# Kernel optimization log

Hardware: AMD Instinct MI355X
Metric: run time of the kernel (lower is better)

## Reference

```python
import math
import jax, jax.numpy as jnp
import numpy as np

CH = 256
NUM_GROUPS = 32
EPS = 1e-5


def setup_inputs() -> dict:
    key = jax.random.key(0)
    ks = jax.random.split(key, 8)
    B, C, S = 32, CH, 32
    x = jax.random.normal(ks[0], (B, C, S, S), dtype=jnp.float32)
    t_embd = jax.random.normal(ks[1], (B, 4 * C), dtype=jnp.float32)
    gamma = jnp.ones((C,), dtype=jnp.float32)
    beta = jnp.zeros((C,), dtype=jnp.float32)
    # torch nn.Linear(ch, 3*ch): weight shape (3*ch, ch), y = x @ W.T + b
    w_attn = jax.random.normal(ks[2], (3 * C, C), dtype=jnp.float32) * (1.0 / math.sqrt(C))
    b_attn = jax.random.normal(ks[3], (3 * C,), dtype=jnp.float32) * 0.02
    w_proj = jax.random.normal(ks[4], (C, C), dtype=jnp.float32) * (1.0 / math.sqrt(C))
    b_proj = jax.random.normal(ks[5], (C,), dtype=jnp.float32) * 0.02
    return {
        "x": x, "t_embd": t_embd,
        "gamma": gamma, "beta": beta,
        "w_attn": w_attn, "b_attn": b_attn,
        "w_proj": w_proj, "b_proj": b_proj,
    }


def _group_norm(x, gamma, beta):
    # x: (B, C, S, S), normalize over (C/G, S, S) per group
    B, C, S, _ = x.shape
    xg = x.reshape(B, NUM_GROUPS, (C // NUM_GROUPS) * S * S)
    mean = jnp.mean(xg, axis=-1, keepdims=True)
    var = jnp.var(xg, axis=-1, keepdims=True)
    xn = ((xg - mean) * jax.lax.rsqrt(var + EPS)).reshape(B, C, S, S)
    return xn * gamma[None, :, None, None] + beta[None, :, None, None]


def reference(x, t_embd, gamma, beta, w_attn, b_attn, w_proj, b_proj):
    B, C, S, _ = x.shape
    norm_x = _group_norm(x, gamma, beta)
    h = jnp.transpose(norm_x, (0, 2, 3, 1))            # (B, S, S, C)
    qkv = h @ w_attn.T + b_attn                        # (B, S, S, 3C)
    q, k, v = jnp.split(qkv, 3, axis=3)
    # full spatial attention: scores over all S*S key positions
    att = jnp.einsum('bhwc,bHWc->bhwHW', q, k) * (1.0 / math.sqrt(C))
    att = jax.nn.softmax(att.reshape(B, S, S, S * S), axis=-1).reshape(B, S, S, S, S)
    o = jnp.einsum('bhwHW,bHWc->bhwc', att, v)         # (B, S, S, C)
    y = o @ w_proj.T + b_proj
    y = jnp.transpose(y, (0, 3, 1, 2))                 # (B, C, S, S)
    return x + y
```

## Files before the change

kernel.cpp:

```cpp
#include <hip/hip_runtime.h>
#include <hip/hip_bf16.h>
#include <stdint.h>
#include <stddef.h>


typedef float  f32x4  __attribute__((ext_vector_type(4)));
typedef __bf16 bf16x8 __attribute__((ext_vector_type(8)));
typedef __bf16 bf16x4 __attribute__((ext_vector_type(4)));

#define DEVI static __device__ __forceinline__

DEVI f32x4 mfma16(bf16x8 a, bf16x8 b, f32x4 c) {
  return __builtin_amdgcn_mfma_f32_16x16x32_bf16(a, b, c, 0, 0, 0);
}

DEVI f32x4 zero4() { f32x4 z = {0.f, 0.f, 0.f, 0.f}; return z; }

typedef const __attribute__((address_space(1))) void* gas_cvp;
typedef __attribute__((address_space(3))) void*       las_vp;

DEVI void gl_lds16(const __bf16* g, __bf16* l) {
  __builtin_amdgcn_global_load_lds((gas_cvp)g, (las_vp)l, 16, 0, 0);
}

__global__ __launch_bounds__(256) void cvt_weights(
    const float* __restrict__ wa, const float* __restrict__ wp,
    __bf16* __restrict__ wab, __bf16* __restrict__ wpb) {
  const int i = blockIdx.x * 256 + threadIdx.x;
  if (i < 196608) {
    wab[i] = (__bf16)wa[i];
  } else {
    const int j = i - 196608;
    if (j < 65536) wpb[j] = (__bf16)wp[j];
  }
}

__global__ __launch_bounds__(256) void gn_stats(
    const float* __restrict__ x, float* __restrict__ mean, float* __restrict__ rstd) {
  const int bg = blockIdx.x;
  const f32x4* base = (const f32x4*)(x + (size_t)bg * 8192);
  float s = 0.f, ss = 0.f;
  for (int i = threadIdx.x; i < 2048; i += 256) {
    f32x4 v = base[i];
    s  += v[0] + v[1] + v[2] + v[3];
    ss += v[0]*v[0] + v[1]*v[1] + v[2]*v[2] + v[3]*v[3];
  }
#pragma unroll
  for (int m = 1; m < 64; m <<= 1) {
    s  += __shfl_xor(s,  m, 64);
    ss += __shfl_xor(ss, m, 64);
  }
  __shared__ float red[8];
  const int lane = threadIdx.x & 63, wave = threadIdx.x >> 6;
  if (lane == 0) { red[wave] = s; red[wave + 4] = ss; }
  __syncthreads();
  if (threadIdx.x == 0) {
    float S  = red[0] + red[1] + red[2] + red[3];
    float SS = red[4] + red[5] + red[6] + red[7];
    float mu  = S * (1.f / 8192.f);
    float var = SS * (1.f / 8192.f) - mu * mu;
    mean[bg] = mu;
    rstd[bg] = rsqrtf(var + 1e-5f);
  }
}

__global__ __launch_bounds__(256) void gn_apply(
    const float* __restrict__ x, const float* __restrict__ mean,
    const float* __restrict__ rstd, const float* __restrict__ gamma,
    const float* __restrict__ beta, __bf16* __restrict__ h) {
  __shared__ __align__(16) __bf16 tile[256 * 64];
  const int b = blockIdx.x >> 4;
  const int p0 = (blockIdx.x & 15) << 6;
  const int tid = threadIdx.x;
#pragma unroll
  for (int it = 0; it < 16; ++it) {
    const int ch = it * 256 + tid;
    const int c = ch >> 4, p4 = ch & 15;
    f32x4 v = *(const f32x4*)(x + (((size_t)(b * 256 + c)) << 10) + p0 + p4 * 4);
    const int bg = b * 32 + (c >> 3);
    const float rs = rstd[bg];
    const float ga = gamma[c] * rs;
    const float be = beta[c] - mean[bg] * ga;
    bf16x4 pk;
#pragma unroll
    for (int r = 0; r < 4; ++r) pk[r] = (__bf16)(v[r] * ga + be);
    *(bf16x4*)((char*)tile + c * 128 + ((p4 * 8) ^ ((c & 7) << 4))) = pk;
  }
  __syncthreads();
  const int p = tid & 63;
#pragma unroll
  for (int it = 0; it < 8; ++it) {
    const int cg = (tid >> 6) * 8 + it;
    bf16x8 vals;
#pragma unroll
    for (int jj = 0; jj < 8; ++jj) {
      const int c = cg * 8 + jj;
      vals[jj] = *(const __bf16*)((const char*)tile + c * 128 + ((p * 2) ^ (jj << 4)));
    }
    *(bf16x8*)(h + (((size_t)(b * 1024 + p0 + p)) << 8) + cg * 8) = vals;
  }
}

DEVI void gemm_core_k256(const __bf16* __restrict__ A0, const __bf16* __restrict__ B0,
                         __bf16* lA, __bf16* lB, int lane, int wave, f32x4 acc[4][4]) {
  const int wm = (wave >> 1) * 64;
  const int wn = (wave & 1) * 64;
  const int r15 = lane & 15, lg = lane >> 4;
#pragma unroll
  for (int i = 0; i < 4; ++i)
#pragma unroll
    for (int j = 0; j < 4; ++j) acc[i][j] = zero4();

  for (int ko = 0; ko < 4; ++ko) {
#pragma unroll
    for (int it = 0; it < 4; ++it) {
      const int q = wave * 256 + it * 64 + lane;
      const int row = q >> 3, c8 = q & 7;
      const int srcoff = row * 256 + ko * 64 + ((c8 ^ (row & 7)) << 3);
      gl_lds16(A0 + srcoff, lA + (size_t)(wave * 256 + it * 64) * 8);
      gl_lds16(B0 + srcoff, lB + (size_t)(wave * 256 + it * 64) * 8);
    }
    __syncthreads();
#pragma unroll
    for (int kk = 0; kk < 2; ++kk) {
      bf16x8 af[4], bfr[4];
#pragma unroll
      for (int i = 0; i < 4; ++i) {
        const int row = wm + i * 16 + r15;
        af[i] = *(const bf16x8*)((const char*)lA + row * 128 +
                                 (((kk * 4 + lg) ^ (row & 7)) << 4));
      }
#pragma unroll
      for (int j = 0; j < 4; ++j) {
        const int row = wn + j * 16 + r15;
        bfr[j] = *(const bf16x8*)((const char*)lB + row * 128 +
                                  (((kk * 4 + lg) ^ (row & 7)) << 4));
      }
#pragma unroll
      for (int i = 0; i < 4; ++i)
#pragma unroll
        for (int j = 0; j < 4; ++j) acc[i][j] = mfma16(af[i], bfr[j], acc[i][j]);
    }
    __syncthreads();
  }
}

__global__ __launch_bounds__(256) void qkv_gemm(
    const __bf16* __restrict__ h, const __bf16* __restrict__ wab,
    const float* __restrict__ b_attn,
    __bf16* __restrict__ q, __bf16* __restrict__ k, __bf16* __restrict__ vt) {
  __shared__ __align__(16) __bf16 lA[128 * 64], lB[128 * 64];
  const int nt = blockIdx.x, mt = blockIdx.y;
  const int tid = threadIdx.x, lane = tid & 63, wave = tid >> 6;
  f32x4 acc[4][4];
  gemm_core_k256(h + (size_t)mt * 128 * 256, wab + (size_t)nt * 128 * 256,
                 lA, lB, lane, wave, acc);

  const int wm = (wave >> 1) * 64, wn = (wave & 1) * 64;
  const int r15 = lane & 15, lg = lane >> 4;
  const int sec = nt >> 1;
  const float QS = 0.0625f * 1.44269504088896340736f;
#pragma unroll
  for (int j = 0; j < 4; ++j) {
    const int ng = nt * 128 + wn + j * 16 + r15;
    const float bias = b_attn[ng];
    const int c = ng & 255;
#pragma unroll
    for (int i = 0; i < 4; ++i) {
      const int mbase = mt * 128 + wm + i * 16 + lg * 4;
      if (sec == 0) {
#pragma unroll
        for (int r = 0; r < 4; ++r)
          q[(size_t)(mbase + r) * 256 + c] = (__bf16)((acc[i][j][r] + bias) * QS);
      } else if (sec == 1) {
#pragma unroll
        for (int r = 0; r < 4; ++r)
          k[(size_t)(mbase + r) * 256 + c] = (__bf16)(acc[i][j][r] + bias);
      } else {
        const int b = mbase >> 10, p = mbase & 1023;
        bf16x4 pk;
#pragma unroll
        for (int r = 0; r < 4; ++r) pk[r] = (__bf16)(acc[i][j][r] + bias);
        *(bf16x4*)(vt + (((size_t)(b * 256 + c)) << 10) + p) = pk;
      }
    }
  }
}

__global__ __launch_bounds__(256, 2) void attn(
    const __bf16* __restrict__ q, const __bf16* __restrict__ k,
    const __bf16* __restrict__ vt, __bf16* __restrict__ o) {
  extern __shared__ __align__(16) char smem[];
  __bf16* lK = (__bf16*)smem;
  __bf16* lV = (__bf16*)(smem + 32768);

  const int bid = blockIdx.x;
  const int xcd = bid & 7, sub = bid >> 3;
  const int b = xcd * 4 + (sub & 3);
  const int qt = sub >> 2;
  const int tid = threadIdx.x, lane = tid & 63, wave = tid >> 6;
  const int r15 = lane & 15, lg = lane >> 4, rs7 = r15 & 7;
  const int m0 = qt * 64 + wave * 16;
  char* P = smem + 65536 + wave * 2048;

  const __bf16* kb = k  + ((size_t)b << 18);
  const __bf16* vb = vt + ((size_t)b << 18);

  const __bf16* qb = q + (((size_t)(b * 1024 + m0)) << 8);
  bf16x8 qf[8];
#pragma unroll
  for (int kc = 0; kc < 8; ++kc)
    qf[kc] = *(const bf16x8*)(qb + ((size_t)r15) * 256 + kc * 32 + lg * 8);

  f32x4 po[16];
#pragma unroll
  for (int d = 0; d < 16; ++d) po[d] = zero4();
  float mrun[4] = {-1e30f, -1e30f, -1e30f, -1e30f};
  float lrun[4] = {0.f, 0.f, 0.f, 0.f};

  auto stageK = [&](int n0) {
#pragma unroll
    for (int it = 0; it < 8; ++it) {
      const int qch = it * 256 + tid;
      const int row = qch >> 5, c32 = qch & 31;
      gl_lds16(kb + (size_t)(n0 + row) * 256 + ((c32 ^ (row & 7)) << 3),
               lK + (size_t)(it * 256 + wave * 64) * 8);
    }
  };
  auto stageV = [&](int n0) {
#pragma unroll
    for (int it = 0; it < 8; ++it) {
      const int qch = it * 256 + tid;
      const int row = qch >> 3, c8 = qch & 7;
      gl_lds16(vb + ((size_t)row << 10) + n0 + ((c8 ^ (row & 7)) << 3),
               lV + (size_t)(it * 256 + wave * 64) * 8);
    }
  };

  stageK(0);
  stageV(0);
  __syncthreads();

  for (int kv = 0; kv < 16; ++kv) {
    const int n0n = (kv + 1) * 64;
    f32x4 s[4];
#pragma unroll
    for (int j = 0; j < 4; ++j) s[j] = zero4();
#pragma unroll
    for (int kc = 0; kc < 8; ++kc) {
      bf16x8 bfr[4];
#pragma unroll
      for (int j = 0; j < 4; ++j)
        bfr[j] = *(const bf16x8*)((const char*)lK + (j * 16 + r15) * 512 +
                                  (((kc * 4 + lg) ^ rs7) << 4));
#pragma unroll
      for (int j = 0; j < 4; ++j) s[j] = mfma16(qf[kc], bfr[j], s[j]);
    }
    float scl[4];
#pragma unroll
    for (int r = 0; r < 4; ++r) {
      float mx = fmaxf(fmaxf(s[0][r], s[1][r]), fmaxf(s[2][r], s[3][r]));
#pragma unroll
      for (int mm = 1; mm < 16; mm <<= 1) mx = fmaxf(mx, __shfl_xor(mx, mm, 64));
      const float mn = fmaxf(mrun[r], mx);
      scl[r] = exp2f(mrun[r] - mn);
      mrun[r] = mn;
    }
#pragma unroll
    for (int j = 0; j < 4; ++j)
#pragma unroll
      for (int r = 0; r < 4; ++r) s[j][r] = exp2f(s[j][r] - mrun[r]);
#pragma unroll
    for (int r = 0; r < 4; ++r) {
      float t = s[0][r] + s[1][r] + s[2][r] + s[3][r];
#pragma unroll
      for (int mm = 1; mm < 16; mm <<= 1) t += __shfl_xor(t, mm, 64);
      lrun[r] = lrun[r] * scl[r] + t;
    }
#pragma unroll
    for (int d = 0; d < 16; ++d)
#pragma unroll
      for (int r = 0; r < 4; ++r) po[d][r] *= scl[r];
#pragma unroll
    for (int j = 0; j < 4; ++j)
#pragma unroll
      for (int r = 0; r < 4; ++r) {
        const int prow = lg * 4 + r;
        *(__bf16*)(P + prow * 128 + (((j * 16 + r15) * 2) ^ ((prow & 7) << 4))) =
            (__bf16)s[j][r];
      }
    __syncthreads();
    if (kv < 15) stageK(n0n);
#pragma unroll
    for (int kk = 0; kk < 2; ++kk) {
      const bf16x8 pa =
          *(const bf16x8*)(P + r15 * 128 + (((kk * 4 + lg) ^ rs7) << 4));
#pragma unroll
      for (int df = 0; df < 16; ++df) {
        const bf16x8 vf = *(const bf16x8*)((const char*)lV + (df * 16 + r15) * 128 +
                                           (((kk * 4 + lg) ^ rs7) << 4));
        po[df] = mfma16(pa, vf, po[df]);
      }
    }
    __syncthreads();
    if (kv < 15) stageV(n0n);
  }
  __bf16* ob = o + (((size_t)(b * 1024 + m0)) << 8);
#pragma unroll
  for (int r = 0; r < 4; ++r) {
    const float inv = 1.f / lrun[r];
#pragma unroll
    for (int df = 0; df < 16; ++df)
      ob[(size_t)(lg * 4 + r) * 256 + df * 16 + r15] = (__bf16)(po[df][r] * inv);
  }
}

__global__ __launch_bounds__(256) void proj_gemm(
    const __bf16* __restrict__ o, const __bf16* __restrict__ wpb,
    const float* __restrict__ b_proj, const float* __restrict__ x,
    float* __restrict__ out) {
  __shared__ __align__(16) __bf16 lA[128 * 64], lB[128 * 64];
  const int nt = blockIdx.x, mt = blockIdx.y;
  const int tid = threadIdx.x, lane = tid & 63, wave = tid >> 6;
  f32x4 acc[4][4];
  gemm_core_k256(o + (size_t)mt * 128 * 256, wpb + (size_t)nt * 128 * 256,
                 lA, lB, lane, wave, acc);

  const int wm = (wave >> 1) * 64, wn = (wave & 1) * 64;
  const int r15 = lane & 15, lg = lane >> 4;
#pragma unroll
  for (int j = 0; j < 4; ++j) {
    const int c = nt * 128 + wn + j * 16 + r15;
    const float bias = b_proj[c];
#pragma unroll
    for (int i = 0; i < 4; ++i) {
      const int mbase = mt * 128 + wm + i * 16 + lg * 4;
      const int b = mbase >> 10, p = mbase & 1023;
      const size_t off = (((size_t)(b * 256 + c)) << 10) + p;
      f32x4 xv = *(const f32x4*)(x + off);
      f32x4 r = acc[i][j];
      r = r + xv;
      r = r + bias;
      *(f32x4*)(out + off) = r;
    }
  }
}

extern "C" void kernel_launch(void* const* d_in, const int* in_sizes, int n_in,
                              void* d_out, int out_size, void* d_ws, size_t ws_size,
                              hipStream_t stream) {
  const float* x      = (const float*)d_in[0];
  const float* gamma  = (const float*)d_in[2];
  const float* beta   = (const float*)d_in[3];
  const float* w_attn = (const float*)d_in[4];
  const float* b_attn = (const float*)d_in[5];
  const float* w_proj = (const float*)d_in[6];
  const float* b_proj = (const float*)d_in[7];
  float* out = (float*)d_out;

  char* ws = (char*)d_ws;
  __bf16* h   = (__bf16*)(ws);
  __bf16* qb  = (__bf16*)(ws + ((size_t)16 << 20));
  __bf16* kb  = (__bf16*)(ws + ((size_t)32 << 20));
  __bf16* vtb = (__bf16*)(ws + ((size_t)48 << 20));
  __bf16* wab = (__bf16*)(ws + ((size_t)64 << 20));
  __bf16* wpb = wab + 196608;
  float*  mean = (float*)(wpb + 65536);
  float*  rstd = mean + 1024;

  cvt_weights<<<1024, 256, 0, stream>>>(w_attn, w_proj, wab, wpb);
  gn_stats<<<1024, 256, 0, stream>>>(x, mean, rstd);
  gn_apply<<<512, 256, 0, stream>>>(x, mean, rstd, gamma, beta, h);
  qkv_gemm<<<dim3(6, 256), 256, 0, stream>>>(h, wab, b_attn, qb, kb, vtb);
  attn<<<512, 256, 73728, stream>>>(qb, kb, vtb, h );
  proj_gemm<<<dim3(2, 256), 256, 0, stream>>>(h, wpb, b_proj, x, out);
}
```

Measured before the change: 140.7 us.

## Fuse group-norm kernels and rework attention with double buffering and lazy rescale

The two group-norm kernels become one. Each block holds its group in LDS, computes the statistics and writes the normalized bf16 output directly. The attention kernel now uses 512 threads and 128 queries per block. It double-buffers K and V through global_load_lds with explicit vmcnt waits and raw barriers, and swaps the MFMA operands to a transposed S^T layout so each lane owns one query row. It also adds a lazy online-softmax rescale that is skipped unless the max grows by more than 8. These changes aim to cut launch overhead, hide load latency and reduce per-iteration softmax shuffles, at the cost of 147KB of LDS per block and correctness that depends on the wait counts.

Result: faster. 131.6 us (-6.5%).

```diff
diff --git a/kernel.cpp b/kernel.cpp
--- a/kernel.cpp
+++ b/kernel.cpp
@@ -21,6 +21,13 @@
 
 DEVI void gl_lds16(const __bf16* g, __bf16* l) {
   __builtin_amdgcn_global_load_lds((gas_cvp)g, (las_vp)l, 16, 0, 0);
+}
+
+#define WAIT_VM(N) asm volatile("s_waitcnt vmcnt(" #N ")" ::: "memory")
+DEVI void bar() {
+  asm volatile("" ::: "memory");
+  __builtin_amdgcn_s_barrier();
+  asm volatile("" ::: "memory");
 }
 
 __global__ __launch_bounds__(256) void cvt_weights(
@@ -35,13 +42,21 @@
   }
 }
 
-__global__ __launch_bounds__(256) void gn_stats(
-    const float* __restrict__ x, float* __restrict__ mean, float* __restrict__ rstd) {
+__global__ __launch_bounds__(256) void gn_fused(
+    const float* __restrict__ x, const float* __restrict__ gamma,
+    const float* __restrict__ beta, __bf16* __restrict__ h) {
+  __shared__ __align__(16) float xs[8192];
+  __shared__ float redS[4], redSS[4];
   const int bg = blockIdx.x;
-  const f32x4* base = (const f32x4*)(x + (size_t)bg * 8192);
+  const int b = bg >> 5, g = bg & 31;
+  const int tid = threadIdx.x;
+  const float* base = x + (size_t)bg * 8192;
   float s = 0.f, ss = 0.f;
-  for (int i = threadIdx.x; i < 2048; i += 256) {
-    f32x4 v = base[i];
+#pragma unroll
+  for (int it = 0; it < 8; ++it) {
+    const int i = it * 256 + tid;
+    f32x4 v = *(const f32x4*)(base + i * 4);
+    *(f32x4*)(xs + i * 4) = v;
     s  += v[0] + v[1] + v[2] + v[3];
     ss += v[0]*v[0] + v[1]*v[1] + v[2]*v[2] + v[3]*v[3];
   }
@@ -50,54 +65,29 @@
     s  += __shfl_xor(s,  m, 64);
     ss += __shfl_xor(ss, m, 64);
   }
-  __shared__ float red[8];
-  const int lane = threadIdx.x & 63, wave = threadIdx.x >> 6;
-  if (lane == 0) { red[wave] = s; red[wave + 4] = ss; }
+  const int lane = tid & 63, wave = tid >> 6;
+  if (lane == 0) { redS[wave] = s; redSS[wave] = ss; }
   __syncthreads();
-  if (threadIdx.x == 0) {
-    float S  = red[0] + red[1] + red[2] + red[3];
-    float SS = red[4] + red[5] + red[6] + red[7];
-    float mu  = S * (1.f / 8192.f);
-    float var = SS * (1.f / 8192.f) - mu * mu;
-    mean[bg] = mu;
-    rstd[bg] = rsqrtf(var + 1e-5f);
-  }
-}
-
-__global__ __launch_bounds__(256) void gn_apply(
-    const float* __restrict__ x, const float* __restrict__ mean,
-    const float* __restrict__ rstd, const float* __restrict__ gamma,
-    const float* __restrict__ beta, __bf16* __restrict__ h) {
-  __shared__ __align__(16) __bf16 tile[256 * 64];
-  const int b = blockIdx.x >> 4;
-  const int p0 = (blockIdx.x & 15) << 6;
-  const int tid = threadIdx.x;
-#pragma unroll
-  for (int it = 0; it < 16; ++it) {
-    const int ch = it * 256 + tid;
-    const int c = ch >> 4, p4 = ch & 15;
-    f32x4 v = *(const f32x4*)(x + (((size_t)(b * 256 + c)) << 10) + p0 + p4 * 4);
-    const int bg = b * 32 + (c >> 3);
-    const float rs = rstd[bg];
-    const float ga = gamma[c] * rs;
-    const float be = beta[c] - mean[bg] * ga;
-    bf16x4 pk;
-#pragma unroll
-    for (int r = 0; r < 4; ++r) pk[r] = (__bf16)(v[r] * ga + be);
-    *(bf16x4*)((char*)tile + c * 128 + ((p4 * 8) ^ ((c & 7) << 4))) = pk;
-  }
-  __syncthreads();
-  const int p = tid & 63;
-#pragma unroll
-  for (int it = 0; it < 8; ++it) {
-    const int cg = (tid >> 6) * 8 + it;
-    bf16x8 vals;
-#pragma unroll
-    for (int jj = 0; jj < 8; ++jj) {
-      const int c = cg * 8 + jj;
-      vals[jj] = *(const __bf16*)((const char*)tile + c * 128 + ((p * 2) ^ (jj << 4)));
-    }
-    *(bf16x8*)(h + (((size_t)(b * 1024 + p0 + p)) << 8) + cg * 8) = vals;
+  const float S  = redS[0] + redS[1] + redS[2] + redS[3];
+  const float SS = redSS[0] + redSS[1] + redSS[2] + redSS[3];
+  const float mu = S * (1.f / 8192.f);
+  const float rstd = rsqrtf(SS * (1.f / 8192.f) - mu * mu + 1e-5f);
+  float ga[8], be[8];
+#pragma unroll
+  for (int j = 0; j < 8; ++j) {
+    const int c = g * 8 + j;
+    ga[j] = gamma[c] * rstd;
+    be[j] = beta[c] - mu * ga[j];
+  }
+  __bf16* hb = h + ((size_t)b << 18) + g * 8;
+#pragma unroll
+  for (int it = 0; it < 4; ++it) {
+    const int p = it * 256 + tid;
+    bf16x8 o8;
+#pragma unroll
+    for (int j = 0; j < 8; ++j)
+      o8[j] = (__bf16)(xs[j * 1024 + p] * ga[j] + be[j]);
+    *(bf16x8*)(hb + ((size_t)p << 8)) = o8;
   }
 }
 
@@ -187,12 +177,10 @@
   }
 }
 
-__global__ __launch_bounds__(256, 2) void attn(
+__global__ __launch_bounds__(512, 2) void attn(
     const __bf16* __restrict__ q, const __bf16* __restrict__ k,
     const __bf16* __restrict__ vt, __bf16* __restrict__ o) {
   extern __shared__ __align__(16) char smem[];
-  __bf16* lK = (__bf16*)smem;
-  __bf16* lV = (__bf16*)(smem + 32768);
 
   const int bid = blockIdx.x;
   const int xcd = bid & 7, sub = bid >> 3;
@@ -200,8 +188,8 @@
   const int qt = sub >> 2;
   const int tid = threadIdx.x, lane = tid & 63, wave = tid >> 6;
   const int r15 = lane & 15, lg = lane >> 4, rs7 = r15 & 7;
-  const int m0 = qt * 64 + wave * 16;
-  char* P = smem + 65536 + wave * 2048;
+  const int m0 = qt * 128 + wave * 16;
+  char* P = smem + 131072 + wave * 2048;
 
   const __bf16* kb = k  + ((size_t)b << 18);
   const __bf16* vb = vt + ((size_t)b << 18);
@@ -215,103 +203,110 @@
   f32x4 po[16];
 #pragma unroll
   for (int d = 0; d < 16; ++d) po[d] = zero4();
-  float mrun[4] = {-1e30f, -1e30f, -1e30f, -1e30f};
-  float lrun[4] = {0.f, 0.f, 0.f, 0.f};
-
-  auto stageK = [&](int n0) {
-#pragma unroll
-    for (int it = 0; it < 8; ++it) {
-      const int qch = it * 256 + tid;
+  float mrun = -1e30f, lrun = 0.f;
+
+  auto stageK = [&](int n0, int buf) {
+    __bf16* dst = (__bf16*)(smem + buf * 32768);
+#pragma unroll
+    for (int it = 0; it < 4; ++it) {
+      const int qch = it * 512 + tid;
       const int row = qch >> 5, c32 = qch & 31;
       gl_lds16(kb + (size_t)(n0 + row) * 256 + ((c32 ^ (row & 7)) << 3),
-               lK + (size_t)(it * 256 + wave * 64) * 8);
+               dst + (size_t)(it * 512 + wave * 64) * 8);
     }
   };
-  auto stageV = [&](int n0) {
-#pragma unroll
-    for (int it = 0; it < 8; ++it) {
-      const int qch = it * 256 + tid;
+  auto stageV = [&](int n0, int buf) {
+    __bf16* dst = (__bf16*)(smem + 65536 + buf * 32768);
+#pragma unroll
+    for (int it = 0; it < 4; ++it) {
+      const int qch = it * 512 + tid;
       const int row = qch >> 3, c8 = qch & 7;
       gl_lds16(vb + ((size_t)row << 10) + n0 + ((c8 ^ (row & 7)) << 3),
-               lV + (size_t)(it * 256 + wave * 64) * 8);
+               dst + (size_t)(it * 512 + wave * 64) * 8);
     }
   };
 
-  stageK(0);
-  stageV(0);
-  __syncthreads();
+  stageK(0, 0);
+  stageV(0, 0);
 
   for (int kv = 0; kv < 16; ++kv) {
-    const int n0n = (kv + 1) * 64;
+    const int cur = kv & 1;
+    const char* lK = (const char*)smem + cur * 32768;
+    const char* lV = (const char*)smem + 65536 + cur * 32768;
+    if (kv < 15) {
+      stageK((kv + 1) * 64, cur ^ 1);
+      stageV((kv + 1) * 64, cur ^ 1);
+      WAIT_VM(8);
+    } else {
+      WAIT_VM(0);
+    }
+    bar();
+
     f32x4 s[4];
 #pragma unroll
     for (int j = 0; j < 4; ++j) s[j] = zero4();
 #pragma unroll
     for (int kc = 0; kc < 8; ++kc) {
-      bf16x8 bfr[4];
+      bf16x8 kf[4];
 #pragma unroll
       for (int j = 0; j < 4; ++j)
-        bfr[j] = *(const bf16x8*)((const char*)lK + (j * 16 + r15) * 512 +
-                                  (((kc * 4 + lg) ^ rs7) << 4));
-#pragma unroll
-      for (int j = 0; j < 4; ++j) s[j] = mfma16(qf[kc], bfr[j], s[j]);
-    }
-    float scl[4];
-#pragma unroll
-    for (int r = 0; r < 4; ++r) {
-      float mx = fmaxf(fmaxf(s[0][r], s[1][r]), fmaxf(s[2][r], s[3][r]));
-#pragma unroll
-      for (int mm = 1; mm < 16; mm <<= 1) mx = fmaxf(mx, __shfl_xor(mx, mm, 64));
-      const float mn = fmaxf(mrun[r], mx);
-      scl[r] = exp2f(mrun[r] - mn);
-      mrun[r] = mn;
-    }
+        kf[j] = *(const bf16x8*)(lK + (j * 16 + r15) * 512 +
+                                 (((kc * 4 + lg) ^ rs7) << 4));
+#pragma unroll
+      for (int j = 0; j < 4; ++j) s[j] = mfma16(kf[j], qf[kc], s[j]);
+    }
+    float pmax = s[0][0];
 #pragma unroll
     for (int j = 0; j < 4; ++j)
 #pragma unroll
-      for (int r = 0; r < 4; ++r) s[j][r] = exp2f(s[j][r] - mrun[r]);
-#pragma unroll
-    for (int r = 0; r < 4; ++r) {
-      float t = s[0][r] + s[1][r] + s[2][r] + s[3][r];
-#pragma unroll
-      for (int mm = 1; mm < 16; mm <<= 1) t += __shfl_xor(t, mm, 64);
-      lrun[r] = lrun[r] * scl[r] + t;
-    }
-#pragma unroll
-    for (int d = 0; d < 16; ++d)
-#pragma unroll
-      for (int r = 0; r < 4; ++r) po[d][r] *= scl[r];
+      for (int r = 0; r < 4; ++r) pmax = fmaxf(pmax, s[j][r]);
+    pmax = fmaxf(pmax, __shfl_xor(pmax, 16, 64));
+    pmax = fmaxf(pmax, __shfl_xor(pmax, 32, 64));
+    if (!__all(pmax <= mrun + 8.f)) {
+      const float mn = fmaxf(mrun, pmax);
+      const float scl = exp2f(mrun - mn);
+      mrun = mn;
+      lrun *= scl;
+#pragma unroll
+      for (int d = 0; d < 16; ++d) po[d] *= scl;
+    }
+    float psum = 0.f;
+    bf16x4 pk[4];
 #pragma unroll
     for (int j = 0; j < 4; ++j)
 #pragma unroll
       for (int r = 0; r < 4; ++r) {
-        const int prow = lg * 4 + r;
-        *(__bf16*)(P + prow * 128 + (((j * 16 + r15) * 2) ^ ((prow & 7) << 4))) =
-            (__bf16)s[j][r];
-      }
-    __syncthreads();
-    if (kv < 15) stageK(n0n);
+        const float pv = exp2f(s[j][r] - mrun);
+        psum += pv;
+        pk[j][r] = (__bf16)pv;
+      }
+    psum += __shfl_xor(psum, 16, 64);
+    psum += __shfl_xor(psum, 32, 64);
+    lrun += psum;
+#pragma unroll
+    for (int j = 0; j < 4; ++j)
+      *(bf16x4*)(P + r15 * 128 + ((j * 32 + lg * 8) ^ (rs7 << 4))) = pk[j];
 #pragma unroll
     for (int kk = 0; kk < 2; ++kk) {
-      const bf16x8 pa =
+      const bf16x8 pb =
           *(const bf16x8*)(P + r15 * 128 + (((kk * 4 + lg) ^ rs7) << 4));
 #pragma unroll
       for (int df = 0; df < 16; ++df) {
-        const bf16x8 vf = *(const bf16x8*)((const char*)lV + (df * 16 + r15) * 128 +
+        const bf16x8 vf = *(const bf16x8*)(lV + (df * 16 + r15) * 128 +
                                            (((kk * 4 + lg) ^ rs7) << 4));
-        po[df] = mfma16(pa, vf, po[df]);
-      }
-    }
-    __syncthreads();
-    if (kv < 15) stageV(n0n);
-  }
-  __bf16* ob = o + (((size_t)(b * 1024 + m0)) << 8);
-#pragma unroll
-  for (int r = 0; r < 4; ++r) {
-    const float inv = 1.f / lrun[r];
-#pragma unroll
-    for (int df = 0; df < 16; ++df)
-      ob[(size_t)(lg * 4 + r) * 256 + df * 16 + r15] = (__bf16)(po[df][r] * inv);
+        po[df] = mfma16(vf, pb, po[df]);
+      }
+    }
+    bar();
+  }
+  const float inv = 1.f / lrun;
+  __bf16* ob = o + (((size_t)(b * 1024 + m0 + r15)) << 8);
+#pragma unroll
+  for (int df = 0; df < 16; ++df) {
+    bf16x4 t;
+#pragma unroll
+    for (int r = 0; r < 4; ++r) t[r] = (__bf16)(po[df][r] * inv);
+    *(bf16x4*)(ob + df * 16 + lg * 4) = t;
   }
 }
 
@@ -365,13 +360,10 @@
   __bf16* vtb = (__bf16*)(ws + ((size_t)48 << 20));
   __bf16* wab = (__bf16*)(ws + ((size_t)64 << 20));
   __bf16* wpb = wab + 196608;
-  float*  mean = (float*)(wpb + 65536);
-  float*  rstd = mean + 1024;
 
   cvt_weights<<<1024, 256, 0, stream>>>(w_attn, w_proj, wab, wpb);
-  gn_stats<<<1024, 256, 0, stream>>>(x, mean, rstd);
-  gn_apply<<<512, 256, 0, stream>>>(x, mean, rstd, gamma, beta, h);
+  gn_fused<<<1024, 256, 0, stream>>>(x, gamma, beta, h);
   qkv_gemm<<<dim3(6, 256), 256, 0, stream>>>(h, wab, b_attn, qb, kb, vtb);
-  attn<<<512, 256, 73728, stream>>>(qb, kb, vtb, h );
+  attn<<<256, 512, 147456, stream>>>(qb, kb, vtb, h );
   proj_gemm<<<dim3(2, 256), 256, 0, stream>>>(h, wpb, b_proj, x, out);
 }
```
